# Kernel optimization log

Measured on AMD Instinct MI355X. Metric: run time of the kernel, lower is better.

The kernel has to match this reference:

```python
import jax, jax.numpy as jnp
import numpy as np

B, S, D, H = 2, 2048, 1024, 16
HD = D // H  # head dim 64
LN_EPS = 1e-12


def setup_inputs() -> dict:
    key = jax.random.key(0)
    ks = jax.random.split(key, 10)
    sc = 0.02
    return {
        "input_tensor": jax.random.normal(ks[0], (B, S, D), dtype=jnp.float32),
        "attention_mask": jnp.zeros((B, 1, 1, S), dtype=jnp.float32),
        "Wq": jax.random.normal(ks[1], (D, D), dtype=jnp.float32) * sc,
        "bq": jnp.zeros((D,), dtype=jnp.float32),
        "Wk": jax.random.normal(ks[2], (D, D), dtype=jnp.float32) * sc,
        "bk": jnp.zeros((D,), dtype=jnp.float32),
        "Wv": jax.random.normal(ks[3], (D, D), dtype=jnp.float32) * sc,
        "bv": jnp.zeros((D,), dtype=jnp.float32),
        "Wo": jax.random.normal(ks[4], (D, D), dtype=jnp.float32) * sc,
        "bo": jnp.zeros((D,), dtype=jnp.float32),
        "ln_gamma": jnp.ones((D,), dtype=jnp.float32),
        "ln_beta": jnp.zeros((D,), dtype=jnp.float32),
    }


def _split_heads(x):
    # [B,S,D] -> [B,H,S,hd]
    return x.reshape(B, S, H, HD).transpose(0, 2, 1, 3)


def reference(input_tensor, attention_mask, Wq, bq, Wk, bk, Wv, bv, Wo, bo, ln_gamma, ln_beta):
    q = _split_heads(input_tensor @ Wq + bq)
    k = _split_heads(input_tensor @ Wk + bk)
    v = _split_heads(input_tensor @ Wv + bv)
    scores = jnp.einsum("bhqd,bhkd->bhqk", q, k) / jnp.sqrt(jnp.float32(HD))
    scores = scores + attention_mask  # additive mask broadcast
    probs = jax.nn.softmax(scores, axis=-1)
    ctx = jnp.einsum("bhqk,bhkd->bhqd", probs, v)
    ctx = ctx.transpose(0, 2, 1, 3).reshape(B, S, D)
    hidden = ctx @ Wo + bo
    x = hidden + input_tensor
    mu = jnp.mean(x, axis=-1, keepdims=True)
    var = jnp.mean(jnp.square(x - mu), axis=-1, keepdims=True)
    return (x - mu) / jnp.sqrt(var + LN_EPS) * ln_gamma + ln_beta
```

## Files before the change

### kernel.cpp

```cpp
#include <hip/hip_runtime.h>
#include <stdint.h>

#define Bb 2
#define Ss 2048
#define Dd 1024
#define Hh 16
#define HD 64
#define Mtot 4096

typedef __bf16 bf16x8 __attribute__((ext_vector_type(8)));
typedef float f32x4 __attribute__((ext_vector_type(4)));
typedef unsigned short ushort_t;

#if __has_builtin(__builtin_amdgcn_exp2f)
#define EXP2(x) __builtin_amdgcn_exp2f(x)
#else
#define EXP2(x) __expf((x) * 0.6931472f)
#endif

__device__ __forceinline__ float bf2f(ushort_t u) {
    union { uint32_t i; float f; } v;
    v.i = ((uint32_t)u) << 16;
    return v.f;
}

__device__ __forceinline__ ushort_t f2bf(float f) {
    union { float f; uint32_t i; } v;
    v.f = f;
    uint32_t u = v.i;
    u += 0x7FFFu + ((u >> 16) & 1u);
    return (ushort_t)(u >> 16);
}

__device__ __forceinline__ uint32_t fbits(float f) {
    union { float f; uint32_t i; } v; v.f = f; return v.i;
}

__device__ __forceinline__ float load_in(const void* p, size_t i, int isf32) {
    if (isf32) return ((const float*)p)[i];
    return bf2f(((const ushort_t*)p)[i]);
}

__device__ __forceinline__ void gload_lds16(const void* g, void* l) {
    __builtin_amdgcn_global_load_lds(
        (const __attribute__((address_space(1))) void*)g,
        (__attribute__((address_space(3))) void*)l, 16, 0, 0);
}

#define NCONV 4204544ull
__global__ __launch_bounds__(256) void prep_k(
    const void* X, const void* mask, const void* bq, const void* bk,
    const void* bv, const void* bo, const void* g, const void* be,
    const void* Wq, const void* Wk, const void* Wv, const void* Wo,
    int* __restrict__ flag, ushort_t* __restrict__ cX,
    ushort_t* __restrict__ cMask, ushort_t* __restrict__ cB,
    ushort_t* __restrict__ wt) {
    __shared__ int sflag;
    __shared__ ushort_t tile[32][33];
    const int tid = threadIdx.x;
    {
        const int lane = tid & 63;
        if (tid < 64) {
            const ushort_t* Xu = (const ushort_t*)X;
            int local = 0;
            for (int i = lane; i < 2048; i += 64) {
                int e = (Xu[i] >> 7) & 0xFF;
                local += (e >= 0x90);
            }
            for (int off = 1; off < 64; off <<= 1) local += __shfl_xor(local, off);
            if (lane == 0) sflag = (local >= 4) ? 1 : 0;
        }
    }
    __syncthreads();
    const int f = sflag;
    if (blockIdx.x == 0 && tid == 0) *flag = f;

    if (blockIdx.x < 1024) {
        const size_t stride = 1024ull * 256ull;
        for (size_t i = (size_t)blockIdx.x * 256 + tid; i < NCONV; i += stride) {
            if (i < 4194304ull) {
                cX[i] = f2bf(load_in(X, i, f));
            } else if (i < 4198400ull) {
                size_t j = i - 4194304ull;
                cMask[j] = f2bf(load_in(mask, j, f));
            } else {
                size_t j = i - 4198400ull;
                int w = (int)(j >> 10);
                size_t r = j & 1023ull;
                const void* p = (w == 0) ? bq : (w == 1) ? bk : (w == 2) ? bv
                              : (w == 3) ? bo : (w == 4) ? g : be;
                cB[w * 1024 + r] = f2bf(load_in(p, r, f));
            }
        }
    } else {
        int id2 = blockIdx.x - 1024;
        int z = id2 >> 10;
        int rem = id2 & 1023;
        int bx = rem & 31, by = rem >> 5;
        const void* W = (z == 0) ? Wq : (z == 1) ? Wk : (z == 2) ? Wv : Wo;
        ushort_t* T = wt + (size_t)z * Dd * Dd;
        int tx = tid & 31, ty = tid >> 5;
        int x = bx * 32 + tx;
        int y0 = by * 32;
        for (int i = 0; i < 4; i++) {
            int y = y0 + ty + i * 8;
            tile[ty + i * 8][tx] = f2bf(load_in(W, (size_t)y * Dd + x, f));
        }
        __syncthreads();
        int x2 = by * 32 + tx;
        int y20 = bx * 32;
        for (int i = 0; i < 4; i++) {
            int y = y20 + ty + i * 8;
            T[(size_t)y * Dd + x2] = tile[tx][ty + i * 8];
        }
    }
}

__global__ __launch_bounds__(256) void gemm_qkv(
    const ushort_t* __restrict__ X, const ushort_t* __restrict__ wt,
    const ushort_t* __restrict__ cB,
    ushort_t* __restrict__ Qb, ushort_t* __restrict__ Kb, ushort_t* __restrict__ Vtb) {
    const int z = blockIdx.z;
    const ushort_t* Wt = wt + (size_t)z * Dd * Dd;
    const ushort_t* bias = cB + z * 1024;

    __shared__ __align__(16) ushort_t smem[2][2][128 * 32];

    const int tid = threadIdx.x;
    const int lane = tid & 63, wv = tid >> 6;
    const int quad = lane >> 4, l15 = lane & 15;
    const int wrow = (wv >> 1) * 64, wcol = (wv & 1) * 64;
    const int row0 = blockIdx.y * 128, col0 = blockIdx.x * 128;
    const int lrow = lane >> 2, lcol = (lane & 3) * 8;

    const f32x4 fzero = {0.f, 0.f, 0.f, 0.f};
    f32x4 acc[4][4];
    for (int mt = 0; mt < 4; mt++)
        for (int nt = 0; nt < 4; nt++) acc[mt][nt] = fzero;

    for (int j = 0; j < 2; j++) {
        int ch = wv * 2 + j;
        gload_lds16(&X[(size_t)(row0 + ch * 16 + lrow) * Dd + lcol],
                    &smem[0][0][ch * 512]);
        gload_lds16(&Wt[(size_t)(col0 + ch * 16 + lrow) * Dd + lcol],
                    &smem[0][1][ch * 512]);
    }

    for (int k0 = 0; k0 < Dd; k0 += 32) {
        const int buf = (k0 >> 5) & 1;
        __syncthreads();
        if (k0 + 32 < Dd) {
            for (int j = 0; j < 2; j++) {
                int ch = wv * 2 + j;
                gload_lds16(&X[(size_t)(row0 + ch * 16 + lrow) * Dd + k0 + 32 + lcol],
                            &smem[buf ^ 1][0][ch * 512]);
                gload_lds16(&Wt[(size_t)(col0 + ch * 16 + lrow) * Dd + k0 + 32 + lcol],
                            &smem[buf ^ 1][1][ch * 512]);
            }
        }
        const ushort_t* As = &smem[buf][0][0];
        const ushort_t* Bs = &smem[buf][1][0];
        bf16x8 af[4], bfr[4];
        for (int mt = 0; mt < 4; mt++)
            af[mt] = *(const bf16x8*)(&As[(wrow + mt * 16 + l15) * 32 + quad * 8]);
        for (int nt = 0; nt < 4; nt++)
            bfr[nt] = *(const bf16x8*)(&Bs[(wcol + nt * 16 + l15) * 32 + quad * 8]);
        for (int mt = 0; mt < 4; mt++)
            for (int nt = 0; nt < 4; nt++)
                acc[mt][nt] = __builtin_amdgcn_mfma_f32_16x16x32_bf16(
                    af[mt], bfr[nt], acc[mt][nt], 0, 0, 0);
    }

    const float qscale = 0.18033688f;
    ushort_t* Cs = &smem[0][0][0];
    for (int mt = 0; mt < 4; mt++) {
        __syncthreads();
        for (int nt = 0; nt < 4; nt++) {
            int gn = col0 + wcol + nt * 16 + l15;
            float bv_ = bf2f(bias[gn]);
            for (int r = 0; r < 4; r++) {
                float v = acc[mt][nt][r] + bv_;
                if (z == 0) v *= qscale;
                int ric = (wv >> 1) * 16 + quad * 4 + r;
                Cs[ric * 136 + wcol + nt * 16 + l15] = f2bf(v);
            }
        }
        __syncthreads();
        if (z == 2) {
            int c = tid >> 1, r0 = (tid & 1) * 16;
            int gn = col0 + c, h = gn >> 6, d = gn & 63;
            int gmbase = row0 + (r0 >> 4) * 64 + mt * 16;
            int b = gmbase >> 11, s0 = gmbase & 2047;
            union { ushort_t u[16]; uint4 q[2]; } pk;
            for (int i = 0; i < 16; i++) pk.u[i] = Cs[(r0 + i) * 136 + c];
            uint4* dst = (uint4*)&Vtb[((size_t)((b * Hh + h) * HD + d)) * Ss + s0];
            dst[0] = pk.q[0];
            dst[1] = pk.q[1];
        } else {
            int ric = tid >> 3, c0 = (tid & 7) * 16;
            int gm = row0 + (ric >> 4) * 64 + mt * 16 + (ric & 15);
            int gn = col0 + c0, h = gn >> 6, d0 = gn & 63;
            int b = gm >> 11, s = gm & 2047;
            const uint4* src = (const uint4*)&Cs[ric * 136 + c0];
            ushort_t* Ob = (z == 0) ? Qb : Kb;
            uint4* dst = (uint4*)&Ob[((size_t)((b * Hh + h) * Ss + s)) * HD + d0];
            dst[0] = src[0];
            dst[1] = src[1];
        }
    }
}

#define STR 36
__global__ __launch_bounds__(512) void attn(
    const ushort_t* __restrict__ Q, const ushort_t* __restrict__ K,
    const ushort_t* __restrict__ Vt, const ushort_t* __restrict__ mask,
    ushort_t* __restrict__ ctx) {
    const int tid = threadIdx.x;
    const int lane = tid & 63, wv = tid >> 6;
    const int quad = lane >> 4, l15 = lane & 15;
    const int bh = blockIdx.x;
    const int b = bh >> 4, h = bh & 15;
    const int q0 = blockIdx.y * 128 + wv * 16;

    const ushort_t* Qh = Q + (size_t)bh * Ss * HD;
    const ushort_t* Kh = K + (size_t)bh * Ss * HD;
    const ushort_t* Vh = Vt + (size_t)bh * HD * Ss;

    __shared__ __align__(16) ushort_t Ks[2][64 * 64];
    __shared__ __align__(16) ushort_t Vs[2][64 * 64];
    __shared__ __align__(16) float maskF[Ss];
    __shared__ __align__(16) ushort_t Pl[8][16 * STR];
    ushort_t* Pw = &Pl[wv][0];

    for (int i = tid; i < Ss; i += 512)
        maskF[i] = (bf2f(mask[b * Ss + i]) - 4.0f) * 1.4426950f;

    const int r8 = lane >> 3, c8 = lane & 7, gc = c8 ^ r8;
    const int sw = l15 & 7;

    gload_lds16(&Kh[(size_t)(wv * 8 + r8) * HD + gc * 8], &Ks[0][wv * 512]);
    gload_lds16(&Vh[(size_t)(wv * 8 + r8) * Ss + gc * 8], &Vs[0][wv * 512]);

    bf16x8 qf[2];
    qf[0] = *(const bf16x8*)(&Qh[(size_t)(q0 + l15) * HD + quad * 8]);
    qf[1] = *(const bf16x8*)(&Qh[(size_t)(q0 + l15) * HD + 32 + quad * 8]);

    bf16x8 onesf;
    {
        union { ushort_t u[8]; bf16x8 v; } ou;
        for (int i = 0; i < 8; i++) ou.u[i] = 0x3F80;
        onesf = ou.v;
    }

    const f32x4 fzero = {0.f, 0.f, 0.f, 0.f};
    f32x4 o[4];
    for (int dt = 0; dt < 4; dt++) o[dt] = fzero;
    f32x4 o_l = fzero;

    for (int kb = 0; kb < Ss; kb += 64) {
        const int buf = (kb >> 6) & 1;
        __syncthreads();

        if (kb + 64 < Ss) {
            gload_lds16(&Kh[(size_t)(kb + 64 + wv * 8 + r8) * HD + gc * 8],
                        &Ks[buf ^ 1][wv * 512]);
            gload_lds16(&Vh[(size_t)(wv * 8 + r8) * Ss + kb + 64 + gc * 8],
                        &Vs[buf ^ 1][wv * 512]);
        }

        const ushort_t* ks = &Ks[buf][0];
        const ushort_t* vs = &Vs[buf][0];

        f32x4 st[4];
        for (int kt = 0; kt < 4; kt++) {
            f32x4 mk = *(const f32x4*)(&maskF[kb + kt * 16 + quad * 4]);
            bf16x8 kf0 = *(const bf16x8*)(&ks[(kt * 16 + l15) * 64 + ((quad) ^ sw) * 8]);
            bf16x8 kf1 = *(const bf16x8*)(&ks[(kt * 16 + l15) * 64 + ((quad + 4) ^ sw) * 8]);
            st[kt] = __builtin_amdgcn_mfma_f32_16x16x32_bf16(kf0, qf[0], mk, 0, 0, 0);
            st[kt] = __builtin_amdgcn_mfma_f32_16x16x32_bf16(kf1, qf[1], st[kt], 0, 0, 0);
        }

        for (int kt = 0; kt < 4; kt++) {
            float e0 = EXP2(st[kt][0]);
            float e1 = EXP2(st[kt][1]);
            float e2 = EXP2(st[kt][2]);
            float e3 = EXP2(st[kt][3]);
            uint2 pk;
            pk.x = __builtin_amdgcn_perm(fbits(e1), fbits(e0), 0x07060302u);
            pk.y = __builtin_amdgcn_perm(fbits(e3), fbits(e2), 0x07060302u);
            *(uint2*)(&Pw[l15 * STR + kt * 16 + quad * 4]) = pk;
        }

        for (int c = 0; c < 2; c++) {
            union { uint2 u2[2]; bf16x8 v; } pu;
            pu.u2[0] = *(const uint2*)(&Pw[l15 * STR + c * 32 + quad * 8]);
            pu.u2[1] = *(const uint2*)(&Pw[l15 * STR + c * 32 + quad * 8 + 4]);
            bf16x8 pf = pu.v;
            for (int dt = 0; dt < 4; dt++) {
                bf16x8 vf = *(const bf16x8*)(
                    &vs[(dt * 16 + l15) * 64 + ((c * 4 + quad) ^ sw) * 8]);
                o[dt] = __builtin_amdgcn_mfma_f32_16x16x32_bf16(pf, vf, o[dt], 0, 0, 0);
            }
            o_l = __builtin_amdgcn_mfma_f32_16x16x32_bf16(pf, onesf, o_l, 0, 0, 0);
        }
    }

    for (int r = 0; r < 4; r++) {
        int q = q0 + quad * 4 + r;
        float linv = 1.f / o_l[r];
        for (int dt = 0; dt < 4; dt++) {
            ctx[((size_t)(b * Ss + q)) * Dd + h * HD + dt * 16 + l15] =
                f2bf(o[dt][r] * linv);
        }
    }
}

__global__ __launch_bounds__(256) void gemm_out(
    const ushort_t* __restrict__ A, const ushort_t* __restrict__ Wt,
    const ushort_t* __restrict__ bo, const ushort_t* __restrict__ X,
    ushort_t* __restrict__ xout) {
    __shared__ __align__(16) ushort_t smem[2][6144];

    const int tid = threadIdx.x;
    const int lane = tid & 63, wv = tid >> 6;
    const int quad = lane >> 4, l15 = lane & 15;
    const int wrow = (wv >> 1) * 32, wcol = (wv & 1) * 64;
    const int row0 = blockIdx.y * 64, col0 = blockIdx.x * 128;
    const int lrow = lane >> 2, lcol = (lane & 3) * 8;

    const f32x4 fzero = {0.f, 0.f, 0.f, 0.f};
    f32x4 acc[2][4];
    for (int mt = 0; mt < 2; mt++)
        for (int nt = 0; nt < 4; nt++) acc[mt][nt] = fzero;

    gload_lds16(&A[(size_t)(row0 + wv * 16 + lrow) * Dd + lcol], &smem[0][wv * 512]);
    for (int j = 0; j < 2; j++) {
        int ch = wv * 2 + j;
        gload_lds16(&Wt[(size_t)(col0 + ch * 16 + lrow) * Dd + lcol],
                    &smem[0][2048 + ch * 512]);
    }

    for (int k0 = 0; k0 < Dd; k0 += 32) {
        const int buf = (k0 >> 5) & 1;
        __syncthreads();
        if (k0 + 32 < Dd) {
            gload_lds16(&A[(size_t)(row0 + wv * 16 + lrow) * Dd + k0 + 32 + lcol],
                        &smem[buf ^ 1][wv * 512]);
            for (int j = 0; j < 2; j++) {
                int ch = wv * 2 + j;
                gload_lds16(&Wt[(size_t)(col0 + ch * 16 + lrow) * Dd + k0 + 32 + lcol],
                            &smem[buf ^ 1][2048 + ch * 512]);
            }
        }
        const ushort_t* As = &smem[buf][0];
        const ushort_t* Bs = &smem[buf][2048];
        bf16x8 af[2], bfr[4];
        for (int mt = 0; mt < 2; mt++)
            af[mt] = *(const bf16x8*)(&As[(wrow + mt * 16 + l15) * 32 + quad * 8]);
        for (int nt = 0; nt < 4; nt++)
            bfr[nt] = *(const bf16x8*)(&Bs[(wcol + nt * 16 + l15) * 32 + quad * 8]);
        for (int mt = 0; mt < 2; mt++)
            for (int nt = 0; nt < 4; nt++)
                acc[mt][nt] = __builtin_amdgcn_mfma_f32_16x16x32_bf16(
                    af[mt], bfr[nt], acc[mt][nt], 0, 0, 0);
    }

    for (int mt = 0; mt < 2; mt++)
        for (int nt = 0; nt < 4; nt++)
            for (int r = 0; r < 4; r++) {
                int gm = row0 + wrow + mt * 16 + quad * 4 + r;
                int gn = col0 + wcol + nt * 16 + l15;
                float v = acc[mt][nt][r] + bf2f(bo[gn]) + bf2f(X[(size_t)gm * Dd + gn]);
                xout[(size_t)gm * Dd + gn] = f2bf(v);
            }
}

__global__ __launch_bounds__(256) void ln_k(
    const ushort_t* __restrict__ x, const ushort_t* __restrict__ gamma,
    const ushort_t* __restrict__ beta, const int* __restrict__ flag,
    void* __restrict__ out) {
    const int row = blockIdx.x;
    const int tid = threadIdx.x;
    const int f = *flag;

    union { uint2 q; ushort_t u[4]; } xv;
    xv.q = ((const uint2*)(x + (size_t)row * Dd))[tid];
    float xi[4];
    for (int i = 0; i < 4; i++) xi[i] = bf2f(xv.u[i]);
    float s = (xi[0] + xi[1]) + (xi[2] + xi[3]);
    float ss = (xi[0] * xi[0] + xi[1] * xi[1]) + (xi[2] * xi[2] + xi[3] * xi[3]);
    for (int off = 1; off < 64; off <<= 1) {
        s += __shfl_xor(s, off);
        ss += __shfl_xor(ss, off);
    }
    __shared__ float ps[4], pss[4];
    int wv = tid >> 6;
    if ((tid & 63) == 0) { ps[wv] = s; pss[wv] = ss; }
    __syncthreads();
    s = ps[0] + ps[1] + ps[2] + ps[3];
    ss = pss[0] + pss[1] + pss[2] + pss[3];
    float mu = s * (1.f / Dd);
    float var = ss * (1.f / Dd) - mu * mu;
    float rstd = rsqrtf(fmaxf(var, 0.f) + 1e-12f);

    const int c0 = tid * 4;
    float r[4];
    for (int i = 0; i < 4; i++) {
        float g = bf2f(gamma[c0 + i]);
        float bb = bf2f(beta[c0 + i]);
        r[i] = (xi[i] - mu) * rstd * g + bb;
    }
    if (f) {
        float4 o4 = {r[0], r[1], r[2], r[3]};
        ((float4*)out)[(size_t)row * 256 + tid] = o4;
    } else {
        union { ushort_t u[4]; uint2 q; } pk;
        for (int i = 0; i < 4; i++) pk.u[i] = f2bf(r[i]);
        *(uint2*)((ushort_t*)out + (size_t)row * Dd + c0) = pk.q;
    }
}

extern "C" void kernel_launch(void* const* d_in, const int* in_sizes, int n_in,
                              void* d_out, int out_size, void* d_ws, size_t ws_size,
                              hipStream_t stream) {
    char* ws = (char*)d_ws;
    int* flag       = (int*)ws;
    ushort_t* cMask = (ushort_t*)(ws + (64ull << 10));
    ushort_t* cB    = (ushort_t*)(ws + (96ull << 10));
    ushort_t* cX    = (ushort_t*)(ws + (1ull << 20));
    ushort_t* wt    = (ushort_t*)(ws + (17ull << 20));
    ushort_t* Qb    = (ushort_t*)(ws + (25ull << 20));
    ushort_t* Kb    = (ushort_t*)(ws + (33ull << 20));
    ushort_t* Vtb   = (ushort_t*)(ws + (41ull << 20));
    ushort_t* ctx   = (ushort_t*)(ws + (49ull << 20));
    ushort_t* xbuf  = (ushort_t*)(ws + (25ull << 20));

    hipLaunchKernelGGL(prep_k, dim3(5120), dim3(256), 0, stream,
                       d_in[0], d_in[1], d_in[3], d_in[5], d_in[7], d_in[9],
                       d_in[10], d_in[11], d_in[2], d_in[4], d_in[6], d_in[8],
                       flag, cX, cMask, cB, wt);
    hipLaunchKernelGGL(gemm_qkv, dim3(8, 32, 3), dim3(256), 0, stream,
                       cX, wt, cB, Qb, Kb, Vtb);
    hipLaunchKernelGGL(attn, dim3(32, 16), dim3(512), 0, stream,
                       Qb, Kb, Vtb, cMask, ctx);
    hipLaunchKernelGGL(gemm_out, dim3(8, 64), dim3(256), 0, stream,
                       ctx, wt + 3ull * Dd * Dd, cB + 3 * 1024, cX, xbuf);
    hipLaunchKernelGGL(ln_k, dim3(Mtot), dim3(256), 0, stream,
                       xbuf, cB + 4 * 1024, cB + 5 * 1024, flag, d_out);
}
```

Before: 210.5 us.

## Split attention over key halves with combine kernel; direct Q/K epilogue stores

Attention is split into two key-range halves via a third grid dimension. Each half writes unnormalized bf16 partial outputs and row sums, and a new combine kernel adds them and normalizes into ctx. This doubles block count to improve CU occupancy, but adds a launch, extra memory traffic, and bf16 rounding of the partial sums. The QKV GEMM epilogue for Q and K now writes scalar bf16 values straight to global memory, dropping the LDS staging and barriers but giving up vectorized stores.

Measured after the change: 225.8 us. +7.3%, slower.

```diff
diff --git a/kernel.cpp b/kernel.cpp
--- a/kernel.cpp
+++ b/kernel.cpp
@@ -172,21 +172,35 @@
     }
 
     const float qscale = 0.18033688f;
-    ushort_t* Cs = &smem[0][0][0];
-    for (int mt = 0; mt < 4; mt++) {
-        __syncthreads();
-        for (int nt = 0; nt < 4; nt++) {
-            int gn = col0 + wcol + nt * 16 + l15;
-            float bv_ = bf2f(bias[gn]);
-            for (int r = 0; r < 4; r++) {
-                float v = acc[mt][nt][r] + bv_;
-                if (z == 0) v *= qscale;
-                int ric = (wv >> 1) * 16 + quad * 4 + r;
-                Cs[ric * 136 + wcol + nt * 16 + l15] = f2bf(v);
-            }
-        }
-        __syncthreads();
-        if (z == 2) {
+    if (z != 2) {
+        ushort_t* Ob = (z == 0) ? Qb : Kb;
+        for (int mt = 0; mt < 4; mt++)
+            for (int nt = 0; nt < 4; nt++) {
+                int gn = col0 + wcol + nt * 16 + l15;
+                int h = gn >> 6, d = gn & 63;
+                float bv_ = bf2f(bias[gn]);
+                for (int r = 0; r < 4; r++) {
+                    int gm = row0 + wrow + mt * 16 + quad * 4 + r;
+                    float v = acc[mt][nt][r] + bv_;
+                    if (z == 0) v *= qscale;
+                    int b = gm >> 11, s = gm & 2047;
+                    Ob[((size_t)((b * Hh + h) * Ss + s)) * HD + d] = f2bf(v);
+                }
+            }
+    } else {
+        ushort_t* Cs = &smem[0][0][0];
+        for (int mt = 0; mt < 4; mt++) {
+            __syncthreads();
+            for (int nt = 0; nt < 4; nt++) {
+                int gn = col0 + wcol + nt * 16 + l15;
+                float bv_ = bf2f(bias[gn]);
+                for (int r = 0; r < 4; r++) {
+                    float v = acc[mt][nt][r] + bv_;
+                    int ric = (wv >> 1) * 16 + quad * 4 + r;
+                    Cs[ric * 136 + wcol + nt * 16 + l15] = f2bf(v);
+                }
+            }
+            __syncthreads();
             int c = tid >> 1, r0 = (tid & 1) * 16;
             int gn = col0 + c, h = gn >> 6, d = gn & 63;
             int gmbase = row0 + (r0 >> 4) * 64 + mt * 16;
@@ -196,50 +210,45 @@
             uint4* dst = (uint4*)&Vtb[((size_t)((b * Hh + h) * HD + d)) * Ss + s0];
             dst[0] = pk.q[0];
             dst[1] = pk.q[1];
-        } else {
-            int ric = tid >> 3, c0 = (tid & 7) * 16;
-            int gm = row0 + (ric >> 4) * 64 + mt * 16 + (ric & 15);
-            int gn = col0 + c0, h = gn >> 6, d0 = gn & 63;
-            int b = gm >> 11, s = gm & 2047;
-            const uint4* src = (const uint4*)&Cs[ric * 136 + c0];
-            ushort_t* Ob = (z == 0) ? Qb : Kb;
-            uint4* dst = (uint4*)&Ob[((size_t)((b * Hh + h) * Ss + s)) * HD + d0];
-            dst[0] = src[0];
-            dst[1] = src[1];
         }
     }
 }
 
 #define STR 36
-__global__ __launch_bounds__(512) void attn(
+#define KHALF 1024
+__global__ __launch_bounds__(512) void attn_part(
     const ushort_t* __restrict__ Q, const ushort_t* __restrict__ K,
     const ushort_t* __restrict__ Vt, const ushort_t* __restrict__ mask,
-    ushort_t* __restrict__ ctx) {
+    ushort_t* __restrict__ o0, ushort_t* __restrict__ o1,
+    float* __restrict__ lpart) {
     const int tid = threadIdx.x;
     const int lane = tid & 63, wv = tid >> 6;
     const int quad = lane >> 4, l15 = lane & 15;
     const int bh = blockIdx.x;
-    const int b = bh >> 4, h = bh & 15;
+    const int b = bh >> 4;
+    const int zz = blockIdx.z;
+    const int kb0 = zz * KHALF;
     const int q0 = blockIdx.y * 128 + wv * 16;
 
     const ushort_t* Qh = Q + (size_t)bh * Ss * HD;
     const ushort_t* Kh = K + (size_t)bh * Ss * HD;
     const ushort_t* Vh = Vt + (size_t)bh * HD * Ss;
+    ushort_t* opart = (zz == 0) ? o0 : o1;
 
     __shared__ __align__(16) ushort_t Ks[2][64 * 64];
     __shared__ __align__(16) ushort_t Vs[2][64 * 64];
-    __shared__ __align__(16) float maskF[Ss];
+    __shared__ __align__(16) float maskF[KHALF];
     __shared__ __align__(16) ushort_t Pl[8][16 * STR];
     ushort_t* Pw = &Pl[wv][0];
 
-    for (int i = tid; i < Ss; i += 512)
-        maskF[i] = (bf2f(mask[b * Ss + i]) - 4.0f) * 1.4426950f;
+    for (int i = tid; i < KHALF; i += 512)
+        maskF[i] = (bf2f(mask[b * Ss + kb0 + i]) - 4.0f) * 1.4426950f;
 
     const int r8 = lane >> 3, c8 = lane & 7, gc = c8 ^ r8;
     const int sw = l15 & 7;
 
-    gload_lds16(&Kh[(size_t)(wv * 8 + r8) * HD + gc * 8], &Ks[0][wv * 512]);
-    gload_lds16(&Vh[(size_t)(wv * 8 + r8) * Ss + gc * 8], &Vs[0][wv * 512]);
+    gload_lds16(&Kh[(size_t)(kb0 + wv * 8 + r8) * HD + gc * 8], &Ks[0][wv * 512]);
+    gload_lds16(&Vh[(size_t)(wv * 8 + r8) * Ss + kb0 + gc * 8], &Vs[0][wv * 512]);
 
     bf16x8 qf[2];
     qf[0] = *(const bf16x8*)(&Qh[(size_t)(q0 + l15) * HD + quad * 8]);
@@ -257,11 +266,12 @@
     for (int dt = 0; dt < 4; dt++) o[dt] = fzero;
     f32x4 o_l = fzero;
 
-    for (int kb = 0; kb < Ss; kb += 64) {
-        const int buf = (kb >> 6) & 1;
+    for (int kk = 0; kk < KHALF; kk += 64) {
+        const int kb = kb0 + kk;
+        const int buf = (kk >> 6) & 1;
         __syncthreads();
 
-        if (kb + 64 < Ss) {
+        if (kk + 64 < KHALF) {
             gload_lds16(&Kh[(size_t)(kb + 64 + wv * 8 + r8) * HD + gc * 8],
                         &Ks[buf ^ 1][wv * 512]);
             gload_lds16(&Vh[(size_t)(wv * 8 + r8) * Ss + kb + 64 + gc * 8],
@@ -273,7 +283,7 @@
 
         f32x4 st[4];
         for (int kt = 0; kt < 4; kt++) {
-            f32x4 mk = *(const f32x4*)(&maskF[kb + kt * 16 + quad * 4]);
+            f32x4 mk = *(const f32x4*)(&maskF[kk + kt * 16 + quad * 4]);
             bf16x8 kf0 = *(const bf16x8*)(&ks[(kt * 16 + l15) * 64 + ((quad) ^ sw) * 8]);
             bf16x8 kf1 = *(const bf16x8*)(&ks[(kt * 16 + l15) * 64 + ((quad + 4) ^ sw) * 8]);
             st[kt] = __builtin_amdgcn_mfma_f32_16x16x32_bf16(kf0, qf[0], mk, 0, 0, 0);
@@ -307,11 +317,41 @@
 
     for (int r = 0; r < 4; r++) {
         int q = q0 + quad * 4 + r;
-        float linv = 1.f / o_l[r];
         for (int dt = 0; dt < 4; dt++) {
-            ctx[((size_t)(b * Ss + q)) * Dd + h * HD + dt * 16 + l15] =
-                f2bf(o[dt][r] * linv);
-        }
+            opart[((size_t)bh * Ss + q) * HD + dt * 16 + l15] = f2bf(o[dt][r]);
+        }
+    }
+    if (l15 == 0) {
+        for (int r = 0; r < 4; r++) {
+            int q = q0 + quad * 4 + r;
+            lpart[(size_t)zz * 65536 + bh * Ss + q] = o_l[r];
+        }
+    }
+}
+
+__global__ __launch_bounds__(256) void combine_k(
+    const ushort_t* __restrict__ o0, const ushort_t* __restrict__ o1,
+    const float* __restrict__ lpart, ushort_t* __restrict__ ctx) {
+    const int bh = blockIdx.x, h = bh & 15, b = bh >> 4;
+    const int tid = threadIdx.x;
+    const int ql = tid >> 1, dh = (tid & 1) * 32;
+    const int q = blockIdx.y * 128 + ql;
+
+    const size_t base = ((size_t)bh * Ss + q) * HD + dh;
+    float l0 = lpart[(size_t)bh * Ss + q];
+    float l1 = lpart[65536ull + bh * Ss + q];
+    float linv = 1.f / (l0 + l1);
+
+    const uint4* p0 = (const uint4*)(o0 + base);
+    const uint4* p1 = (const uint4*)(o1 + base);
+    uint4* pd = (uint4*)(ctx + ((size_t)(b * Ss + q)) * Dd + h * HD + dh);
+    for (int j = 0; j < 4; j++) {
+        union { uint4 q4; ushort_t u[8]; } a, c, r;
+        a.q4 = p0[j];
+        c.q4 = p1[j];
+        for (int i = 0; i < 8; i++)
+            r.u[i] = f2bf((bf2f(a.u[i]) + bf2f(c.u[i])) * linv);
+        pd[j] = r.q4;
     }
 }
 
@@ -427,12 +467,15 @@
     int* flag       = (int*)ws;
     ushort_t* cMask = (ushort_t*)(ws + (64ull << 10));
     ushort_t* cB    = (ushort_t*)(ws + (96ull << 10));
+    float* lpart    = (float*)(ws + (512ull << 10));
     ushort_t* cX    = (ushort_t*)(ws + (1ull << 20));
+    ushort_t* o1b   = (ushort_t*)(ws + (9ull << 20));
     ushort_t* wt    = (ushort_t*)(ws + (17ull << 20));
     ushort_t* Qb    = (ushort_t*)(ws + (25ull << 20));
     ushort_t* Kb    = (ushort_t*)(ws + (33ull << 20));
     ushort_t* Vtb   = (ushort_t*)(ws + (41ull << 20));
-    ushort_t* ctx   = (ushort_t*)(ws + (49ull << 20));
+    ushort_t* o0b   = (ushort_t*)(ws + (49ull << 20));
+    ushort_t* ctx   = (ushort_t*)(ws + (57ull << 20));
     ushort_t* xbuf  = (ushort_t*)(ws + (25ull << 20));
 
     hipLaunchKernelGGL(prep_k, dim3(5120), dim3(256), 0, stream,
@@ -441,8 +484,10 @@
                        flag, cX, cMask, cB, wt);
     hipLaunchKernelGGL(gemm_qkv, dim3(8, 32, 3), dim3(256), 0, stream,
                        cX, wt, cB, Qb, Kb, Vtb);
-    hipLaunchKernelGGL(attn, dim3(32, 16), dim3(512), 0, stream,
-                       Qb, Kb, Vtb, cMask, ctx);
+    hipLaunchKernelGGL(attn_part, dim3(32, 16, 2), dim3(512), 0, stream,
+                       Qb, Kb, Vtb, cMask, o0b, o1b, lpart);
+    hipLaunchKernelGGL(combine_k, dim3(32, 16), dim3(256), 0, stream,
+                       o0b, o1b, lpart, ctx);
     hipLaunchKernelGGL(gemm_out, dim3(8, 64), dim3(256), 0, stream,
                        ctx, wt + 3ull * Dd * Dd, cB + 3 * 1024, cX, xbuf);
     hipLaunchKernelGGL(ln_k, dim3(Mtot), dim3(256), 0, stream,
```
